# Performance work log

Hardware: AMD Instinct MI355X
Metric: run time of the kernel (lower is better)

## Reference

```python
import jax, jax.numpy as jnp
import numpy as np

M, B, N, D, DFF, DCOND = 8, 8, 2048, 512, 2048, 512


def setup_inputs() -> dict:
    key = jax.random.key(0)
    ks = jax.random.split(key, 8)
    s = 0.02  # weight init scale
    return {
        "x": jax.random.normal(ks[0], (B, N, D), dtype=jnp.float32),
        "cond": jax.random.normal(ks[1], (B, DCOND), dtype=jnp.float32),
        "route": jax.random.randint(ks[2], (B,), 0, M, dtype=jnp.int64),
        "W_cond": jax.random.normal(ks[3], (M, DCOND, 2 * D), dtype=jnp.float32) * s,
        "b_cond": jnp.zeros((M, 2 * D), dtype=jnp.float32),
        "W1": jax.random.normal(ks[4], (M, D, DFF), dtype=jnp.float32) * s,
        "b1": jnp.zeros((M, DFF), dtype=jnp.float32),
        "W2": jax.random.normal(ks[5], (M, DFF, D), dtype=jnp.float32) * s,
        "b2": jnp.zeros((M, D), dtype=jnp.float32),
    }


def reference(x, cond, route, W_cond, b_cond, W1, b1, W2, b2):
    # --- all branches computed densely (faithful to the torch module) ---
    # cond modulation per branch: [M, B, 2D]
    mod = jnp.einsum('bc,mcd->mbd', cond, W_cond) + b_cond[:, None, :]
    scale, shift = jnp.split(mod, 2, axis=-1)            # each [M, B, D]
    # FiLM modulate tokens: [M, B, N, D]
    x_mod = x[None] * (1.0 + scale[:, :, None, :]) + shift[:, :, None, :]
    # MLP per branch
    h = jax.nn.gelu(jnp.einsum('mbnd,mdf->mbnf', x_mod, W1) + b1[:, None, None, :])
    stacked = jnp.einsum('mbnf,mfd->mbnd', h, W2) + b2[:, None, None, :]  # [M,B,N,D]
    # --- one-hot select (torch.einsum('mbnd,bm->bnd', stacked, one_hot)) ---
    one_hot = jax.nn.one_hot(route, M, dtype=stacked.dtype)  # [B, M]
    return jnp.einsum('mbnd,bm->bnd', stacked, one_hot)
```

## Files before the change

kernel.cpp:

```cpp
#include <hip/hip_runtime.h>
#include <hip/hip_bf16.h>
#include <cstdint>
#include <cstddef>

#define NEXP   8
#define BATCH  8
#define NTOK   2048
#define DDIM   512
#define DFFDIM 2048
#define DCOND  512

typedef float  f32x4  __attribute__((ext_vector_type(4)));
typedef __bf16 bf16x8 __attribute__((ext_vector_type(8)));

using as1_cvoid = __attribute__((address_space(1))) const void;
using as3_void  = __attribute__((address_space(3))) void;

__device__ __forceinline__ void async_copy16(const void* g, void* l) {
  __builtin_amdgcn_global_load_lds((as1_cvoid*)g, (as3_void*)l, 16, 0, 0);
}

__device__ __forceinline__ unsigned short f2bf_bits(float f) {
  __hip_bfloat16 h = __float2bfloat16(f);
  return *reinterpret_cast<unsigned short*>(&h);
}

__device__ __forceinline__ float gelu_fast(float v) {
  float y = v * fmaf(0.0713548162726f, v * v, 1.5957691216057f);
  float e = exp2f(-1.44269504089f * y);
  return v * __builtin_amdgcn_rcpf(1.0f + e);
}

__global__ void mod_kernel(const float* __restrict__ cond,
                           const int* __restrict__ route,
                           const float* __restrict__ W_cond,
                           const float* __restrict__ b_cond,
                           float* __restrict__ ss) {
  const int b = blockIdx.y;
  const int m = route[b];
  const int tj = threadIdx.x & 63;
  const int cq = threadIdx.x >> 6;
  const int j = blockIdx.x * 64 + tj;
  const float* wc = W_cond + (size_t)m * DCOND * (2 * DDIM);
  const float* cb = cond + (size_t)b * DCOND;
  float acc = 0.f;
#pragma unroll 4
  for (int c = cq * 128; c < cq * 128 + 128; ++c)
    acc += cb[c] * wc[(size_t)c * (2 * DDIM) + j];
  __shared__ float red[4][64];
  red[cq][tj] = acc;
  __syncthreads();
  if (cq == 0) {
    float v = red[0][tj] + red[1][tj] + red[2][tj] + red[3][tj];
    ss[(size_t)b * (2 * DDIM) + j] = v + b_cond[(size_t)m * (2 * DDIM) + j];
  }
}

__global__ void film_kernel(const float* __restrict__ x,
                            const float* __restrict__ ss,
                            __hip_bfloat16* __restrict__ xmod) {
  const size_t idx = (size_t)blockIdx.x * blockDim.x + threadIdx.x;
  const int d4 = (int)(idx & (DDIM / 4 - 1));
  const int b  = (int)(idx >> 18);
  const float4 xv = reinterpret_cast<const float4*>(x)[idx];
  const float4 sc = reinterpret_cast<const float4*>(ss + (size_t)b * 1024)[d4];
  const float4 sh = reinterpret_cast<const float4*>(ss + (size_t)b * 1024 + DDIM)[d4];
  float r0 = xv.x * (1.f + sc.x) + sh.x;
  float r1 = xv.y * (1.f + sc.y) + sh.y;
  float r2 = xv.z * (1.f + sc.z) + sh.z;
  float r3 = xv.w * (1.f + sc.w) + sh.w;
  ushort4 ov;
  ov.x = f2bf_bits(r0); ov.y = f2bf_bits(r1);
  ov.z = f2bf_bits(r2); ov.w = f2bf_bits(r3);
  reinterpret_cast<ushort4*>(xmod)[idx] = ov;
}

__global__ void transpose_cvt(const float* __restrict__ in,
                              __hip_bfloat16* __restrict__ outp,
                              int L, int R,
                              const int* __restrict__ route) {
  const int mi = blockIdx.z;
  bool used = false;
#pragma unroll
  for (int b = 0; b < BATCH; ++b) used |= (route[b] == mi);
  if (!used) return;

  __shared__ float tile[32][33];
  const float* inm = in + (size_t)mi * L * R;
  __hip_bfloat16* outm = outp + (size_t)mi * L * R;
  const int r0 = blockIdx.x * 32, l0 = blockIdx.y * 32;
  const int tx = threadIdx.x, ty = threadIdx.y;
#pragma unroll
  for (int i = 0; i < 32; i += 8)
    tile[ty + i][tx] = inm[(size_t)(l0 + ty + i) * R + r0 + tx];
  __syncthreads();
#pragma unroll
  for (int i = 0; i < 32; i += 8)
    outm[(size_t)(r0 + ty + i) * L + l0 + tx] = __float2bfloat16(tile[tx][ty + i]);
}

template <int EPI>
__global__ __launch_bounds__(512, 1) void gemm_pipe3(
    const __hip_bfloat16* __restrict__ Abase,
    const __hip_bfloat16* __restrict__ Btbase,
    const float* __restrict__ biasbase,
    void* __restrict__ outbase,
    const int* __restrict__ route,
    int Mdim, int Ndim, int Kdim, int tilesX) {
  const int bid  = blockIdx.x;
  const int b    = bid & 7;
  const int tile = bid >> 3;
  const int bx   = tile % tilesX;
  const int by   = tile / tilesX;
  const int m = route[b];
  const __hip_bfloat16* A  = Abase  + (size_t)b * Mdim * Kdim;
  const __hip_bfloat16* Bt = Btbase + (size_t)m * Ndim * Kdim;
  const float* bias = biasbase + (size_t)m * Ndim;
  const int r0 = bx * 256;
  const int n0 = by * 128;

  __shared__ alignas(16) __hip_bfloat16 As[3][256 * 64];
  __shared__ alignas(16) __hip_bfloat16 Bs[3][128 * 64];

  const int t = threadIdx.x;
  const int w = t >> 6, l = t & 63;
  const int wm = w >> 2, wn = w & 3;

  const int srow = t >> 3;
  const int scol = (t & 7) ^ ((t >> 3) & 7);

#define STAGE(s_, k0)                                                         \
  { _Pragma("unroll")                                                         \
    for (int i = 0; i < 4; ++i)                                               \
      async_copy16(A + (size_t)(r0 + i * 64 + srow) * Kdim + (k0) + scol * 8, \
                   &As[s_][(i * 512 + w * 64) * 8]);                          \
    _Pragma("unroll")                                                         \
    for (int i = 0; i < 2; ++i)                                               \
      async_copy16(Bt + (size_t)(n0 + i * 64 + srow) * Kdim + (k0) + scol * 8,\
                   &Bs[s_][(i * 512 + w * 64) * 8]); }

  const int lrow = l & 15, lq = l >> 4, lx = l & 7;
  const int abase = (wm * 128 + lrow) * 8;
  const int bbase = (wn * 32 + lrow) * 8;
  const int swz0 = (lq) ^ lx;
  const int swz1 = (4 + lq) ^ lx;

  f32x4 acc[8][2] = {};
  const int nt = Kdim >> 6;

  STAGE(0, 0)
  STAGE(1, 64)

  int s = 0;
  for (int kt = 0; kt < nt; ++kt) {
    if (kt + 1 < nt) asm volatile("s_waitcnt vmcnt(6)" ::: "memory");
    else             asm volatile("s_waitcnt vmcnt(0)" ::: "memory");
    __builtin_amdgcn_s_barrier();
    __builtin_amdgcn_sched_barrier(0);

    int s2 = s + 2; if (s2 >= 3) s2 -= 3;
    if (kt + 2 < nt) STAGE(s2, (kt + 2) * 64)

    const __hip_bfloat16* as_ = As[s];
    const __hip_bfloat16* bs_ = Bs[s];
    bf16x8 af[8][2], bfr[2][2];
#pragma unroll
    for (int nb = 0; nb < 2; ++nb) {
      bfr[nb][0] = *reinterpret_cast<const bf16x8*>(&bs_[(bbase + nb * 128 + swz0) * 8]);
      bfr[nb][1] = *reinterpret_cast<const bf16x8*>(&bs_[(bbase + nb * 128 + swz1) * 8]);
    }
#pragma unroll
    for (int mb = 0; mb < 8; ++mb) {
      af[mb][0] = *reinterpret_cast<const bf16x8*>(&as_[(abase + mb * 128 + swz0) * 8]);
      af[mb][1] = *reinterpret_cast<const bf16x8*>(&as_[(abase + mb * 128 + swz1) * 8]);
    }
#pragma unroll
    for (int mb = 0; mb < 8; ++mb)
#pragma unroll
      for (int nb = 0; nb < 2; ++nb) {
        acc[mb][nb] = __builtin_amdgcn_mfma_f32_16x16x32_bf16(
            af[mb][0], bfr[nb][0], acc[mb][nb], 0, 0, 0);
        acc[mb][nb] = __builtin_amdgcn_mfma_f32_16x16x32_bf16(
            af[mb][1], bfr[nb][1], acc[mb][nb], 0, 0, 0);
      }

    ++s; if (s == 3) s = 0;
  }
#undef STAGE

  if (EPI == 0) {
    __hip_bfloat16* out = (__hip_bfloat16*)outbase + (size_t)b * Mdim * Ndim;
#pragma unroll
    for (int mb = 0; mb < 8; ++mb) {
      const int row = r0 + wm * 128 + mb * 16 + lq * 4;
#pragma unroll
      for (int nb = 0; nb < 2; ++nb) {
        const int col = n0 + wn * 32 + nb * 16 + lrow;
        const float bv = bias[col];
#pragma unroll
        for (int j = 0; j < 4; ++j) {
          float g = gelu_fast(acc[mb][nb][j] + bv);
          out[(size_t)(row + j) * Ndim + col] = __float2bfloat16(g);
        }
      }
    }
  } else {
    float* out = (float*)outbase + (size_t)b * Mdim * Ndim;
#pragma unroll
    for (int mb = 0; mb < 8; ++mb) {
      const int row = r0 + wm * 128 + mb * 16 + lq * 4;
#pragma unroll
      for (int nb = 0; nb < 2; ++nb) {
        const int col = n0 + wn * 32 + nb * 16 + lrow;
        const float bv = bias[col];
#pragma unroll
        for (int j = 0; j < 4; ++j)
          out[(size_t)(row + j) * Ndim + col] = acc[mb][nb][j] + bv;
      }
    }
  }
}

extern "C" void kernel_launch(void* const* d_in, const int* in_sizes, int n_in,
                              void* d_out, int out_size, void* d_ws, size_t ws_size,
                              hipStream_t stream) {
  const float* x      = (const float*)d_in[0];
  const float* cond   = (const float*)d_in[1];
  const int*   route  = (const int*)d_in[2];
  const float* W_cond = (const float*)d_in[3];
  const float* b_cond = (const float*)d_in[4];
  const float* W1     = (const float*)d_in[5];
  const float* b1     = (const float*)d_in[6];
  const float* W2     = (const float*)d_in[7];
  const float* b2     = (const float*)d_in[8];
  float* out = (float*)d_out;

  const size_t SS_OFF   = 0;
  const size_t XMOD_OFF = 32768;
  const size_t W1T_OFF  = XMOD_OFF + (size_t)BATCH * NTOK * DDIM * 2;
  const size_t W2T_OFF  = W1T_OFF + (size_t)NEXP * DDIM * DFFDIM * 2;
  const size_t H_OFF    = W2T_OFF + (size_t)NEXP * DFFDIM * DDIM * 2;
  const size_t NEED     = H_OFF + (size_t)BATCH * NTOK * DFFDIM * 2;
  if (ws_size < NEED) return;

  char* ws = (char*)d_ws;
  float* ss            = (float*)(ws + SS_OFF);
  __hip_bfloat16* xmod = (__hip_bfloat16*)(ws + XMOD_OFF);
  __hip_bfloat16* w1t  = (__hip_bfloat16*)(ws + W1T_OFF);
  __hip_bfloat16* w2t  = (__hip_bfloat16*)(ws + W2T_OFF);
  __hip_bfloat16* h    = (__hip_bfloat16*)(ws + H_OFF);

  mod_kernel<<<dim3(2 * DDIM / 64, BATCH), 256, 0, stream>>>(cond, route, W_cond, b_cond, ss);

  {
    const size_t groups = (size_t)BATCH * NTOK * DDIM / 4;
    film_kernel<<<(unsigned)(groups / 256), 256, 0, stream>>>(x, ss, xmod);
  }

  transpose_cvt<<<dim3(DFFDIM / 32, DDIM / 32, NEXP), dim3(32, 8), 0, stream>>>(W1, w1t, DDIM, DFFDIM, route);
  transpose_cvt<<<dim3(DDIM / 32, DFFDIM / 32, NEXP), dim3(32, 8), 0, stream>>>(W2, w2t, DFFDIM, DDIM, route);

  gemm_pipe3<0><<<(NTOK / 256) * (DFFDIM / 128) * BATCH, 512, 0, stream>>>(
      xmod, w1t, b1, h, route, NTOK, DFFDIM, DDIM, NTOK / 256);

  gemm_pipe3<1><<<(NTOK / 256) * (DDIM / 128) * BATCH, 512, 0, stream>>>(
      h, w2t, b2, out, route, NTOK, DDIM, DFFDIM, NTOK / 256);
}
```

Before: 152.3 us.

## Switch GEMMs to 128x128 tiles with double buffering and 256-thread blocks

Replaces the 256x128-tile, 512-thread, triple-buffered GEMM with a 128x128-tile, 256-thread, double-buffered version. Each block now uses 2x2 waves holding 64x64 sub-tiles, and launch bounds are set to allow two blocks per CU. The aim is more blocks, better occupancy and better load balance across CUs, especially for the smaller second GEMM. In exchange, each block reuses less data per tile, the prefetch depth drops to one stage, and an extra barrier per k-step is needed to protect the buffer being overwritten.

```diff
diff --git a/kernel.cpp b/kernel.cpp
--- a/kernel.cpp
+++ b/kernel.cpp
@@ -100,7 +100,7 @@
 }
 
 template <int EPI>
-__global__ __launch_bounds__(512, 1) void gemm_pipe3(
+__global__ __launch_bounds__(256, 2) void gemm_db2(
     const __hip_bfloat16* __restrict__ Abase,
     const __hip_bfloat16* __restrict__ Btbase,
     const float* __restrict__ biasbase,
@@ -116,15 +116,15 @@
   const __hip_bfloat16* A  = Abase  + (size_t)b * Mdim * Kdim;
   const __hip_bfloat16* Bt = Btbase + (size_t)m * Ndim * Kdim;
   const float* bias = biasbase + (size_t)m * Ndim;
-  const int r0 = bx * 256;
+  const int r0 = bx * 128;
   const int n0 = by * 128;
 
-  __shared__ alignas(16) __hip_bfloat16 As[3][256 * 64];
-  __shared__ alignas(16) __hip_bfloat16 Bs[3][128 * 64];
+  __shared__ alignas(16) __hip_bfloat16 As[2][128 * 64];
+  __shared__ alignas(16) __hip_bfloat16 Bs[2][128 * 64];
 
   const int t = threadIdx.x;
   const int w = t >> 6, l = t & 63;
-  const int wm = w >> 2, wn = w & 3;
+  const int wr = w >> 1, wc = w & 1;
 
   const int srow = t >> 3;
   const int scol = (t & 7) ^ ((t >> 3) & 7);
@@ -132,70 +132,68 @@
 #define STAGE(s_, k0)                                                         \
   { _Pragma("unroll")                                                         \
     for (int i = 0; i < 4; ++i)                                               \
-      async_copy16(A + (size_t)(r0 + i * 64 + srow) * Kdim + (k0) + scol * 8, \
-                   &As[s_][(i * 512 + w * 64) * 8]);                          \
+      async_copy16(A + (size_t)(r0 + i * 32 + srow) * Kdim + (k0) + scol * 8, \
+                   &As[s_][(i * 256 + t) * 8]);                               \
     _Pragma("unroll")                                                         \
-    for (int i = 0; i < 2; ++i)                                               \
-      async_copy16(Bt + (size_t)(n0 + i * 64 + srow) * Kdim + (k0) + scol * 8,\
-                   &Bs[s_][(i * 512 + w * 64) * 8]); }
+    for (int i = 0; i < 4; ++i)                                               \
+      async_copy16(Bt + (size_t)(n0 + i * 32 + srow) * Kdim + (k0) + scol * 8,\
+                   &Bs[s_][(i * 256 + t) * 8]); }
 
   const int lrow = l & 15, lq = l >> 4, lx = l & 7;
-  const int abase = (wm * 128 + lrow) * 8;
-  const int bbase = (wn * 32 + lrow) * 8;
-  const int swz0 = (lq) ^ lx;
-  const int swz1 = (4 + lq) ^ lx;
-
-  f32x4 acc[8][2] = {};
+  f32x4 acc[4][4] = {};
   const int nt = Kdim >> 6;
 
   STAGE(0, 0)
-  STAGE(1, 64)
-
-  int s = 0;
+
   for (int kt = 0; kt < nt; ++kt) {
-    if (kt + 1 < nt) asm volatile("s_waitcnt vmcnt(6)" ::: "memory");
-    else             asm volatile("s_waitcnt vmcnt(0)" ::: "memory");
+    const int s = kt & 1;
+    if (kt + 1 < nt) {
+      STAGE(s ^ 1, (kt + 1) * 64)
+      asm volatile("s_waitcnt vmcnt(8)" ::: "memory");
+    } else {
+      asm volatile("s_waitcnt vmcnt(0)" ::: "memory");
+    }
     __builtin_amdgcn_s_barrier();
     __builtin_amdgcn_sched_barrier(0);
 
-    int s2 = s + 2; if (s2 >= 3) s2 -= 3;
-    if (kt + 2 < nt) STAGE(s2, (kt + 2) * 64)
-
     const __hip_bfloat16* as_ = As[s];
     const __hip_bfloat16* bs_ = Bs[s];
-    bf16x8 af[8][2], bfr[2][2];
-#pragma unroll
-    for (int nb = 0; nb < 2; ++nb) {
-      bfr[nb][0] = *reinterpret_cast<const bf16x8*>(&bs_[(bbase + nb * 128 + swz0) * 8]);
-      bfr[nb][1] = *reinterpret_cast<const bf16x8*>(&bs_[(bbase + nb * 128 + swz1) * 8]);
-    }
-#pragma unroll
-    for (int mb = 0; mb < 8; ++mb) {
-      af[mb][0] = *reinterpret_cast<const bf16x8*>(&as_[(abase + mb * 128 + swz0) * 8]);
-      af[mb][1] = *reinterpret_cast<const bf16x8*>(&as_[(abase + mb * 128 + swz1) * 8]);
-    }
-#pragma unroll
-    for (int mb = 0; mb < 8; ++mb)
-#pragma unroll
-      for (int nb = 0; nb < 2; ++nb) {
+    bf16x8 af[4][2], bfr[4][2];
+#pragma unroll
+    for (int mb = 0; mb < 4; ++mb) {
+      const int row = wr * 64 + mb * 16 + lrow;
+      af[mb][0] = *reinterpret_cast<const bf16x8*>(&as_[(row * 8 + ((0 + lq) ^ lx)) * 8]);
+      af[mb][1] = *reinterpret_cast<const bf16x8*>(&as_[(row * 8 + ((4 + lq) ^ lx)) * 8]);
+    }
+#pragma unroll
+    for (int nb = 0; nb < 4; ++nb) {
+      const int row = wc * 64 + nb * 16 + lrow;
+      bfr[nb][0] = *reinterpret_cast<const bf16x8*>(&bs_[(row * 8 + ((0 + lq) ^ lx)) * 8]);
+      bfr[nb][1] = *reinterpret_cast<const bf16x8*>(&bs_[(row * 8 + ((4 + lq) ^ lx)) * 8]);
+    }
+#pragma unroll
+    for (int mb = 0; mb < 4; ++mb)
+#pragma unroll
+      for (int nb = 0; nb < 4; ++nb) {
         acc[mb][nb] = __builtin_amdgcn_mfma_f32_16x16x32_bf16(
             af[mb][0], bfr[nb][0], acc[mb][nb], 0, 0, 0);
         acc[mb][nb] = __builtin_amdgcn_mfma_f32_16x16x32_bf16(
             af[mb][1], bfr[nb][1], acc[mb][nb], 0, 0, 0);
       }
 
-    ++s; if (s == 3) s = 0;
+    __builtin_amdgcn_sched_barrier(0);
+    __builtin_amdgcn_s_barrier();
   }
 #undef STAGE
 
   if (EPI == 0) {
     __hip_bfloat16* out = (__hip_bfloat16*)outbase + (size_t)b * Mdim * Ndim;
 #pragma unroll
-    for (int mb = 0; mb < 8; ++mb) {
-      const int row = r0 + wm * 128 + mb * 16 + lq * 4;
-#pragma unroll
-      for (int nb = 0; nb < 2; ++nb) {
-        const int col = n0 + wn * 32 + nb * 16 + lrow;
+    for (int mb = 0; mb < 4; ++mb) {
+      const int row = r0 + wr * 64 + mb * 16 + lq * 4;
+#pragma unroll
+      for (int nb = 0; nb < 4; ++nb) {
+        const int col = n0 + wc * 64 + nb * 16 + lrow;
         const float bv = bias[col];
 #pragma unroll
         for (int j = 0; j < 4; ++j) {
@@ -207,11 +205,11 @@
   } else {
     float* out = (float*)outbase + (size_t)b * Mdim * Ndim;
 #pragma unroll
-    for (int mb = 0; mb < 8; ++mb) {
-      const int row = r0 + wm * 128 + mb * 16 + lq * 4;
-#pragma unroll
-      for (int nb = 0; nb < 2; ++nb) {
-        const int col = n0 + wn * 32 + nb * 16 + lrow;
+    for (int mb = 0; mb < 4; ++mb) {
+      const int row = r0 + wr * 64 + mb * 16 + lq * 4;
+#pragma unroll
+      for (int nb = 0; nb < 4; ++nb) {
+        const int col = n0 + wc * 64 + nb * 16 + lrow;
         const float bv = bias[col];
 #pragma unroll
         for (int j = 0; j < 4; ++j)
@@ -260,9 +258,9 @@
   transpose_cvt<<<dim3(DFFDIM / 32, DDIM / 32, NEXP), dim3(32, 8), 0, stream>>>(W1, w1t, DDIM, DFFDIM, route);
   transpose_cvt<<<dim3(DDIM / 32, DFFDIM / 32, NEXP), dim3(32, 8), 0, stream>>>(W2, w2t, DFFDIM, DDIM, route);
 
-  gemm_pipe3<0><<<(NTOK / 256) * (DFFDIM / 128) * BATCH, 512, 0, stream>>>(
-      xmod, w1t, b1, h, route, NTOK, DFFDIM, DDIM, NTOK / 256);
-
-  gemm_pipe3<1><<<(NTOK / 256) * (DDIM / 128) * BATCH, 512, 0, stream>>>(
-      h, w2t, b2, out, route, NTOK, DDIM, DFFDIM, NTOK / 256);
-}
+  gemm_db2<0><<<(NTOK / 128) * (DFFDIM / 128) * BATCH, 256, 0, stream>>>(
+      xmod, w1t, b1, h, route, NTOK, DFFDIM, DDIM, NTOK / 128);
+
+  gemm_db2<1><<<(NTOK / 128) * (DDIM / 128) * BATCH, 256, 0, stream>>>(
+      h, w2t, b2, out, route, NTOK, DDIM, DFFDIM, NTOK / 128);
+}
```

Result: faster. 137.2 us (-9.9%).
